# Kernel tuning notes

Measured on AMD Instinct MI355X. Metric: run time of the kernel, lower is better.

Reference implementation:

```python
import jax, jax.numpy as jnp
import numpy as np

C_Z = 128
C_H = 128
EPS = 1e-5


def _layer_norm(x, gamma, beta):
    mu = jnp.mean(x, axis=-1, keepdims=True)
    var = jnp.mean(jnp.square(x - mu), axis=-1, keepdims=True)
    return (x - mu) * jax.lax.rsqrt(var + EPS) * gamma + beta


def setup_inputs() -> dict:
    key = jax.random.key(0)
    ks = jax.random.split(key, 8)
    B, N = 1, 512
    s_z = 1.0 / np.sqrt(C_Z)
    s_h = 1.0 / np.sqrt(C_H)
    return {
        "z": jax.random.normal(ks[0], (B, N, N, C_Z), dtype=jnp.float32),
        "mask": jnp.ones((B, N, N), dtype=jnp.float32),
        # linear_ab_p: c_z -> 2*c_hidden
        "w_ab_p": jax.random.normal(ks[1], (2 * C_H, C_Z), dtype=jnp.float32) * s_z,
        "b_ab_p": jnp.zeros((2 * C_H,), dtype=jnp.float32),
        # linear_ab_g: c_z -> 2*c_hidden (gating init)
        "w_ab_g": jax.random.normal(ks[2], (2 * C_H, C_Z), dtype=jnp.float32) * s_z,
        "b_ab_g": jnp.ones((2 * C_H,), dtype=jnp.float32),
        # linear_g: c_z -> c_z (gating init)
        "w_g": jax.random.normal(ks[3], (C_Z, C_Z), dtype=jnp.float32) * s_z,
        "b_g": jnp.ones((C_Z,), dtype=jnp.float32),
        # linear_z: c_hidden -> c_z (final init)
        "w_z": jax.random.normal(ks[4], (C_Z, C_H), dtype=jnp.float32) * s_h,
        "b_z": jnp.zeros((C_Z,), dtype=jnp.float32),
        # layer norms
        "ln_in_g": jnp.ones((C_Z,), dtype=jnp.float32),
        "ln_in_b": jnp.zeros((C_Z,), dtype=jnp.float32),
        "ln_out_g": jnp.ones((C_H,), dtype=jnp.float32),
        "ln_out_b": jnp.zeros((C_H,), dtype=jnp.float32),
    }


def reference(z, mask, w_ab_p, b_ab_p, w_ab_g, b_ab_g, w_g, b_g, w_z, b_z,
              ln_in_g, ln_in_b, ln_out_g, ln_out_b):
    # [B, N, N, C] pair representation; outgoing triangle update
    zn = _layer_norm(z, ln_in_g, ln_in_b)
    m = mask[..., None]  # [B, N, N, 1]
    # gated dual projections: sigmoid(W_g z) * mask * (W_p z)  -> [B, N, N, 2H]
    gate = jax.nn.sigmoid(jnp.einsum("bijc,hc->bijh", zn, w_ab_g) + b_ab_g) * m
    ab = gate * (jnp.einsum("bijc,hc->bijh", zn, w_ab_p) + b_ab_p)
    a, b = jnp.split(ab, 2, axis=-1)  # each [B, N, N, H]
    # outgoing: x[b,i,j,h] = sum_k a[b,i,k,h] * b[b,j,k,h]
    x = jnp.einsum("bikh,bjkh->bijh", a, b)
    x = _layer_norm(x, ln_out_g, ln_out_b)
    out = (jnp.einsum("bijh,ch->bijc", x, w_z) + b_z)
    g = jax.nn.sigmoid(jnp.einsum("bijc,dc->bijd", zn, w_g) + b_g)
    return out * g
```

## Files before the change

### kernel.cpp

```cpp
#include <hip/hip_runtime.h>
#include <math.h>

#define NN 512
#define RR 262144
#define EPS_F 1e-5f

typedef unsigned short u16;
typedef unsigned int u32;
typedef __bf16 bf16x8 __attribute__((ext_vector_type(8)));
typedef float f32x4 __attribute__((ext_vector_type(4)));

__device__ __forceinline__ u16 f2bs(float f) {
  __bf16 h = (__bf16)f;
  return __builtin_bit_cast(u16, h);
}
__device__ __forceinline__ float bs2f(u16 u) {
  return (float)__builtin_bit_cast(__bf16, u);
}
__device__ __forceinline__ float sigmoidf_(float x) {
  return 1.f / (1.f + __expf(-x));
}

__global__ __launch_bounds__(256) void k_wconv(const float* __restrict__ w_ab_p,
                                               const float* __restrict__ w_ab_g,
                                               const float* __restrict__ w_g,
                                               u16* __restrict__ wb) {
  const int u = blockIdx.x * 256 + threadIdx.x;
  const int lane = u & 63;
  const int tl = lane & 15, quad = lane >> 4;
  const int ks = (u >> 6) & 3, nt = (u >> 8) & 3;
  const int wn = (u >> 10) & 1, tt = u >> 11;
  const int n = wn * 64 + nt * 16 + tl;
  const int k = ks * 32 + quad * 8;
  const float* src;
  if (tt < 4) {
    const int srow = tt * 64 + ((n >> 5) << 4) + (n & 15);
    src = (((n >> 4) & 1) ? w_ab_g : w_ab_p) + srow * 128 + k;
  } else {
    src = w_g + n * 128 + k;
  }
  const float4 v0 = *(const float4*)src;
  const float4 v1 = *(const float4*)(src + 4);
  u16 o[8] = {f2bs(v0.x), f2bs(v0.y), f2bs(v0.z), f2bs(v0.w),
              f2bs(v1.x), f2bs(v1.y), f2bs(v1.z), f2bs(v1.w)};
  *(uint4*)(wb + (long)u * 8) = *(uint4*)o;
}

__global__ __launch_bounds__(256, 3) void k_proj(
    const float* __restrict__ z, const float* __restrict__ mask,
    const u16* __restrict__ wb, const float* __restrict__ b_ab_p,
    const float* __restrict__ b_ab_g, const float* __restrict__ b_g,
    const float* __restrict__ ln_g, const float* __restrict__ ln_b,
    u16* __restrict__ a_t, u16* __restrict__ b_t, u16* __restrict__ g_out) {
  __shared__ __align__(16) u16 As[128 * 136];
  __shared__ __align__(16) u16 Ts[64 * 136];
  __shared__ float maskS[128];
  const int t = threadIdx.x;
  const long row0 = (long)blockIdx.x * 128;

  {
    const int row = t >> 1, half = t & 1;
    const float* zr = z + (row0 + row) * 128 + half * 64;
    float vals[64];
    float s = 0.f, sq = 0.f;
#pragma unroll
    for (int i = 0; i < 16; ++i) {
      const float4 v = *(const float4*)(zr + i * 4);
      vals[i * 4 + 0] = v.x;
      vals[i * 4 + 1] = v.y;
      vals[i * 4 + 2] = v.z;
      vals[i * 4 + 3] = v.w;
      s += v.x + v.y + v.z + v.w;
      sq += v.x * v.x + v.y * v.y + v.z * v.z + v.w * v.w;
    }
    s += __shfl_xor(s, 1);
    sq += __shfl_xor(sq, 1);
    const float mu = s * 0.0078125f;
    const float var = sq * 0.0078125f - mu * mu;
    const float rs = rsqrtf(var + EPS_F);
    u16 ob[64];
#pragma unroll
    for (int i = 0; i < 16; ++i) {
      const float4 gg = *(const float4*)(ln_g + half * 64 + i * 4);
      const float4 bb = *(const float4*)(ln_b + half * 64 + i * 4);
      ob[i * 4 + 0] = f2bs((vals[i * 4 + 0] - mu) * rs * gg.x + bb.x);
      ob[i * 4 + 1] = f2bs((vals[i * 4 + 1] - mu) * rs * gg.y + bb.y);
      ob[i * 4 + 2] = f2bs((vals[i * 4 + 2] - mu) * rs * gg.z + bb.z);
      ob[i * 4 + 3] = f2bs((vals[i * 4 + 3] - mu) * rs * gg.w + bb.w);
    }
    uint4* dst = (uint4*)(As + row * 136 + half * 64);
    const uint4* sp = (const uint4*)ob;
#pragma unroll
    for (int i = 0; i < 8; ++i) dst[i] = sp[i];
  }
  if (t < 128) maskS[t] = mask[row0 + t];
  __syncthreads();

  const int lane = t & 63, wv = t >> 6;
  const int quad = lane >> 4, tl = lane & 15;
  const int wm = wv >> 1, wn = wv & 1;

  for (int tt = 0; tt < 5; ++tt) {
    bf16x8 bfr[4][4];
    {
      const u16* wsrc = wb + (tt * 2 + wn) * 8192 + lane * 8;
#pragma unroll
      for (int nt = 0; nt < 4; ++nt)
#pragma unroll
        for (int ks = 0; ks < 4; ++ks)
          bfr[nt][ks] = *(const bf16x8*)(wsrc + (nt * 4 + ks) * 512);
    }

    f32x4 acc[4][4];
#pragma unroll
    for (int mt = 0; mt < 4; ++mt)
#pragma unroll
      for (int nt = 0; nt < 4; ++nt) acc[mt][nt] = (f32x4){0.f, 0.f, 0.f, 0.f};

#pragma unroll
    for (int ks = 0; ks < 4; ++ks) {
      bf16x8 af[4];
#pragma unroll
      for (int mt = 0; mt < 4; ++mt)
        af[mt] = *(const bf16x8*)(As + (wm * 64 + mt * 16 + tl) * 136 + ks * 32 + quad * 8);
#pragma unroll
      for (int mt = 0; mt < 4; ++mt)
#pragma unroll
        for (int nt = 0; nt < 4; ++nt)
          acc[mt][nt] = __builtin_amdgcn_mfma_f32_16x16x32_bf16(af[mt], bfr[nt][ks], acc[mt][nt], 0, 0, 0);
    }

    if (tt < 4) {
      __syncthreads();
#pragma unroll
      for (int b2 = 0; b2 < 2; ++b2) {
        const int hl = wn * 32 + b2 * 16 + tl;
        const int hg = tt * 64 + hl;
        const float bp = b_ab_p[hg], bg = b_ab_g[hg];
#pragma unroll
        for (int mt = 0; mt < 4; ++mt)
#pragma unroll
          for (int rg = 0; rg < 4; ++rg) {
            const int r = wm * 64 + mt * 16 + quad * 4 + rg;
            const float p = acc[mt][2 * b2][rg] + bp;
            const float gt = acc[mt][2 * b2 + 1][rg] + bg;
            Ts[hl * 136 + r] = f2bs(sigmoidf_(gt) * maskS[r] * p);
          }
      }
      __syncthreads();
      {
        const int hl = t >> 2, qq = t & 3;
        const int hg = tt * 64 + hl;
        u16* dbuf = (tt < 2) ? a_t : b_t;
        const int hb = (tt < 2) ? hg : hg - 128;
        const uint4* src = (const uint4*)(Ts + hl * 136 + qq * 32);
        uint4* dst = (uint4*)(dbuf + (long)hb * RR + row0 + qq * 32);
#pragma unroll
        for (int i = 0; i < 4; ++i) dst[i] = src[i];
      }
    } else {
#pragma unroll
      for (int nt = 0; nt < 4; ++nt) {
        const int c = wn * 64 + nt * 16 + tl;
        const float bgc = b_g[c];
#pragma unroll
        for (int mt = 0; mt < 4; ++mt)
#pragma unroll
          for (int rg = 0; rg < 4; ++rg) {
            const int r = wm * 64 + mt * 16 + quad * 4 + rg;
            g_out[(row0 + r) * (long)128 + c] = f2bs(sigmoidf_(acc[mt][nt][rg] + bgc));
          }
      }
    }
  }
}

__global__ __launch_bounds__(256) void k_tri(const u16* __restrict__ a_t,
                                             const u16* __restrict__ b_t,
                                             u16* __restrict__ x_t) {
  __shared__ __align__(16) u16 As[128 * 72];
  __shared__ __align__(16) u16 Bs[128 * 72];
  const int t = threadIdx.x;
  const int h = blockIdx.y;
  const int i0 = (blockIdx.x >> 2) * 128, j0 = (blockIdx.x & 3) * 128;
  const u16* Ag = a_t + (long)h * RR;
  const u16* Bg = b_t + (long)h * RR;
  const int lane = t & 63, wv = t >> 6;
  const int quad = lane >> 4, tl = lane & 15;
  const int wm = wv >> 1, wn = wv & 1;
  const int chunk = t & 7, rb = t >> 3;

  f32x4 acc[4][4];
#pragma unroll
  for (int mt = 0; mt < 4; ++mt)
#pragma unroll
    for (int nt = 0; nt < 4; ++nt) acc[mt][nt] = (f32x4){0.f, 0.f, 0.f, 0.f};

  for (int kt = 0; kt < 8; ++kt) {
    __syncthreads();
#pragma unroll
    for (int p = 0; p < 4; ++p) {
      const int row = rb + p * 32;
      *(uint4*)(As + row * 72 + chunk * 8) =
          *(const uint4*)(Ag + (long)(i0 + row) * 512 + kt * 64 + chunk * 8);
      *(uint4*)(Bs + row * 72 + chunk * 8) =
          *(const uint4*)(Bg + (long)(j0 + row) * 512 + kt * 64 + chunk * 8);
    }
    __syncthreads();
#pragma unroll
    for (int ks = 0; ks < 2; ++ks) {
      bf16x8 af[4], bfr[4];
#pragma unroll
      for (int mt = 0; mt < 4; ++mt)
        af[mt] = *(const bf16x8*)(As + (wm * 64 + mt * 16 + tl) * 72 + ks * 32 + quad * 8);
#pragma unroll
      for (int nt = 0; nt < 4; ++nt)
        bfr[nt] = *(const bf16x8*)(Bs + (wn * 64 + nt * 16 + tl) * 72 + ks * 32 + quad * 8);
#pragma unroll
      for (int mt = 0; mt < 4; ++mt)
#pragma unroll
        for (int nt = 0; nt < 4; ++nt)
          acc[mt][nt] = __builtin_amdgcn_mfma_f32_16x16x32_bf16(af[mt], bfr[nt], acc[mt][nt], 0, 0, 0);
    }
  }
#pragma unroll
  for (int mt = 0; mt < 4; ++mt)
#pragma unroll
    for (int nt = 0; nt < 4; ++nt)
#pragma unroll
      for (int rg = 0; rg < 4; ++rg) {
        const int i = i0 + wm * 64 + mt * 16 + quad * 4 + rg;
        const int j = j0 + wn * 64 + nt * 16 + tl;
        x_t[(long)h * RR + (long)i * 512 + j] = f2bs(acc[mt][nt][rg]);
      }
}

__global__ __launch_bounds__(256) void k_out(const u16* __restrict__ x_t,
                                             const float* __restrict__ w_z,
                                             const float* __restrict__ b_z,
                                             const float* __restrict__ ln_g,
                                             const float* __restrict__ ln_b,
                                             const u16* __restrict__ g_in,
                                             float* __restrict__ out) {
  __shared__ __align__(16) u16 Xs[128 * 136];
  __shared__ __align__(16) u16 Ws[128 * 136];
  __shared__ float lnGs[128], lnBs[128];
  const int t = threadIdx.x;
  const long row0 = (long)blockIdx.x * 128;

  if (t < 128) {
    lnGs[t] = ln_g[t];
    lnBs[t] = ln_b[t];
  }
  {
    const int hb = t >> 3, rq = t & 7;
    u32 xv[4][8];
#pragma unroll
    for (int hh = 0; hh < 4; ++hh) {
      const uint4* src = (const uint4*)(x_t + (long)(hb * 4 + hh) * RR + row0 + rq * 16);
      const uint4 a = src[0], b = src[1];
      xv[hh][0] = a.x; xv[hh][1] = a.y; xv[hh][2] = a.z; xv[hh][3] = a.w;
      xv[hh][4] = b.x; xv[hh][5] = b.y; xv[hh][6] = b.z; xv[hh][7] = b.w;
    }
#pragma unroll
    for (int rr = 0; rr < 16; ++rr) {
      const int wi = rr >> 1, sh = (rr & 1) * 16;
      const u32 e0 = (xv[0][wi] >> sh) & 0xffffu;
      const u32 e1 = (xv[1][wi] >> sh) & 0xffffu;
      const u32 e2 = (xv[2][wi] >> sh) & 0xffffu;
      const u32 e3 = (xv[3][wi] >> sh) & 0xffffu;
      *(uint2*)(Xs + (rq * 16 + rr) * 136 + hb * 4) = make_uint2(e0 | (e1 << 16), e2 | (e3 << 16));
    }
  }
  {
    const int n = t >> 1, half = t & 1;
    const float* src = w_z + n * 128 + half * 64;
    u16* dst = Ws + n * 136 + half * 64;
#pragma unroll
    for (int i = 0; i < 16; ++i) {
      const float4 v = *(const float4*)(src + i * 4);
      dst[i * 4 + 0] = f2bs(v.x);
      dst[i * 4 + 1] = f2bs(v.y);
      dst[i * 4 + 2] = f2bs(v.z);
      dst[i * 4 + 3] = f2bs(v.w);
    }
  }
  __syncthreads();
  {
    const int r = t >> 1, half = t & 1;
    u16* xr = Xs + r * 136 + half * 64;
    float vals[64];
    float s = 0.f, sq = 0.f;
#pragma unroll
    for (int i = 0; i < 64; ++i) {
      const float v = bs2f(xr[i]);
      vals[i] = v;
      s += v;
      sq += v * v;
    }
    s += __shfl_xor(s, 1);
    sq += __shfl_xor(sq, 1);
    const float mu = s * 0.0078125f;
    const float var = sq * 0.0078125f - mu * mu;
    const float rs = rsqrtf(var + EPS_F);
#pragma unroll
    for (int i = 0; i < 64; ++i) {
      const int hh = half * 64 + i;
      xr[i] = f2bs((vals[i] - mu) * rs * lnGs[hh] + lnBs[hh]);
    }
  }
  __syncthreads();

  const int lane = t & 63, wv = t >> 6;
  const int quad = lane >> 4, tl = lane & 15;
  const int wm = wv >> 1, wn = wv & 1;
  f32x4 acc[4][4];
#pragma unroll
  for (int mt = 0; mt < 4; ++mt)
#pragma unroll
    for (int nt = 0; nt < 4; ++nt) acc[mt][nt] = (f32x4){0.f, 0.f, 0.f, 0.f};

#pragma unroll
  for (int ks = 0; ks < 4; ++ks) {
    bf16x8 af[4], bfr[4];
#pragma unroll
    for (int mt = 0; mt < 4; ++mt)
      af[mt] = *(const bf16x8*)(Xs + (wm * 64 + mt * 16 + tl) * 136 + ks * 32 + quad * 8);
#pragma unroll
    for (int nt = 0; nt < 4; ++nt)
      bfr[nt] = *(const bf16x8*)(Ws + (wn * 64 + nt * 16 + tl) * 136 + ks * 32 + quad * 8);
#pragma unroll
    for (int mt = 0; mt < 4; ++mt)
#pragma unroll
      for (int nt = 0; nt < 4; ++nt)
        acc[mt][nt] = __builtin_amdgcn_mfma_f32_16x16x32_bf16(af[mt], bfr[nt], acc[mt][nt], 0, 0, 0);
  }
#pragma unroll
  for (int nt = 0; nt < 4; ++nt) {
    const int c = wn * 64 + nt * 16 + tl;
    const float bz = b_z[c];
#pragma unroll
    for (int mt = 0; mt < 4; ++mt)
#pragma unroll
      for (int rg = 0; rg < 4; ++rg) {
        const int r = wm * 64 + mt * 16 + quad * 4 + rg;
        const long idx = (row0 + r) * 128 + c;
        out[idx] = (acc[mt][nt][rg] + bz) * bs2f(g_in[idx]);
      }
  }
}

extern "C" void kernel_launch(void* const* d_in, const int* in_sizes, int n_in,
                              void* d_out, int out_size, void* d_ws, size_t ws_size,
                              hipStream_t stream) {
  const float* z = (const float*)d_in[0];
  const float* mask = (const float*)d_in[1];
  const float* w_ab_p = (const float*)d_in[2];
  const float* b_ab_p = (const float*)d_in[3];
  const float* w_ab_g = (const float*)d_in[4];
  const float* b_ab_g = (const float*)d_in[5];
  const float* w_g = (const float*)d_in[6];
  const float* b_g = (const float*)d_in[7];
  const float* w_z = (const float*)d_in[8];
  const float* b_z = (const float*)d_in[9];
  const float* ln_in_g = (const float*)d_in[10];
  const float* ln_in_b = (const float*)d_in[11];
  const float* ln_out_g = (const float*)d_in[12];
  const float* ln_out_b = (const float*)d_in[13];
  float* out = (float*)d_out;

  u16* a_t = (u16*)d_ws;
  u16* b_t = a_t + (size_t)RR * 128;
  u16* x_t = b_t + (size_t)RR * 128;
  u16* g_b = x_t + (size_t)RR * 128;
  u16* wb = g_b + (size_t)RR * 128;

  k_wconv<<<40, 256, 0, stream>>>(w_ab_p, w_ab_g, w_g, wb);
  k_proj<<<RR / 128, 256, 0, stream>>>(z, mask, wb, b_ab_p, b_ab_g, b_g,
                                       ln_in_g, ln_in_b, a_t, b_t, g_b);
  k_tri<<<dim3(16, 128), 256, 0, stream>>>(a_t, b_t, x_t);
  k_out<<<RR / 128, 256, 0, stream>>>(x_t, w_z, b_z, ln_out_g, ln_out_b, g_b, out);
}
```

Before: 493.2 us.

## Switch to fp16 MFMA, use direct global-to-LDS loads with XOR swizzle in triangle kernel

Result: no change. 491.9 us (-0.3%).

```diff
diff --git a/kernel.cpp b/kernel.cpp
--- a/kernel.cpp
+++ b/kernel.cpp
@@ -7,42 +7,57 @@
 
 typedef unsigned short u16;
 typedef unsigned int u32;
-typedef __bf16 bf16x8 __attribute__((ext_vector_type(8)));
+typedef _Float16 f16;
+typedef f16 f16x8 __attribute__((ext_vector_type(8)));
 typedef float f32x4 __attribute__((ext_vector_type(4)));
 
-__device__ __forceinline__ u16 f2bs(float f) {
-  __bf16 h = (__bf16)f;
+__device__ __forceinline__ u16 f2hs(float f) {
+  f16 h = (f16)f;
   return __builtin_bit_cast(u16, h);
 }
-__device__ __forceinline__ float bs2f(u16 u) {
-  return (float)__builtin_bit_cast(__bf16, u);
+__device__ __forceinline__ float hs2f(u16 u) {
+  return (float)__builtin_bit_cast(f16, u);
 }
 __device__ __forceinline__ float sigmoidf_(float x) {
   return 1.f / (1.f + __expf(-x));
+}
+__device__ __forceinline__ void gload_lds16(const void* g, void* l) {
+  __builtin_amdgcn_global_load_lds((const __attribute__((address_space(1))) void*)g,
+                                   (__attribute__((address_space(3))) void*)l, 16, 0, 0);
 }
 
 __global__ __launch_bounds__(256) void k_wconv(const float* __restrict__ w_ab_p,
                                                const float* __restrict__ w_ab_g,
                                                const float* __restrict__ w_g,
+                                               const float* __restrict__ w_z,
                                                u16* __restrict__ wb) {
   const int u = blockIdx.x * 256 + threadIdx.x;
-  const int lane = u & 63;
-  const int tl = lane & 15, quad = lane >> 4;
-  const int ks = (u >> 6) & 3, nt = (u >> 8) & 3;
-  const int wn = (u >> 10) & 1, tt = u >> 11;
-  const int n = wn * 64 + nt * 16 + tl;
-  const int k = ks * 32 + quad * 8;
   const float* src;
-  if (tt < 4) {
-    const int srow = tt * 64 + ((n >> 5) << 4) + (n & 15);
-    src = (((n >> 4) & 1) ? w_ab_g : w_ab_p) + srow * 128 + k;
+  if (u < 10240) {
+    const int lane = u & 63;
+    const int tl = lane & 15, quad = lane >> 4;
+    const int ks = (u >> 6) & 3, nt = (u >> 8) & 3;
+    const int wn = (u >> 10) & 1, tt = u >> 11;
+    const int n = wn * 64 + nt * 16 + tl;
+    const int k = ks * 32 + quad * 8;
+    if (tt < 4) {
+      const int srow = tt * 64 + ((n >> 5) << 4) + (n & 15);
+      src = (((n >> 4) & 1) ? w_ab_g : w_ab_p) + srow * 128 + k;
+    } else {
+      src = w_g + n * 128 + k;
+    }
   } else {
-    src = w_g + n * 128 + k;
+    const int u2 = u - 10240;
+    const int lane = u2 & 63;
+    const int ks = (u2 >> 6) & 3, nt = (u2 >> 8) & 3, wn = (u2 >> 10) & 1;
+    const int n = wn * 64 + nt * 16 + (lane & 15);
+    const int k = ks * 32 + (lane >> 4) * 8;
+    src = w_z + n * 128 + k;
   }
   const float4 v0 = *(const float4*)src;
   const float4 v1 = *(const float4*)(src + 4);
-  u16 o[8] = {f2bs(v0.x), f2bs(v0.y), f2bs(v0.z), f2bs(v0.w),
-              f2bs(v1.x), f2bs(v1.y), f2bs(v1.z), f2bs(v1.w)};
+  u16 o[8] = {f2hs(v0.x), f2hs(v0.y), f2hs(v0.z), f2hs(v0.w),
+              f2hs(v1.x), f2hs(v1.y), f2hs(v1.z), f2hs(v1.w)};
   *(uint4*)(wb + (long)u * 8) = *(uint4*)o;
 }
 
@@ -62,7 +77,7 @@
     const int row = t >> 1, half = t & 1;
     const float* zr = z + (row0 + row) * 128 + half * 64;
     float vals[64];
-    float s = 0.f, sq = 0.f;
+    float s = 0.f;
 #pragma unroll
     for (int i = 0; i < 16; ++i) {
       const float4 v = *(const float4*)(zr + i * 4);
@@ -71,22 +86,26 @@
       vals[i * 4 + 2] = v.z;
       vals[i * 4 + 3] = v.w;
       s += v.x + v.y + v.z + v.w;
-      sq += v.x * v.x + v.y * v.y + v.z * v.z + v.w * v.w;
     }
     s += __shfl_xor(s, 1);
+    const float mu = s * 0.0078125f;
+    float sq = 0.f;
+#pragma unroll
+    for (int i = 0; i < 64; ++i) {
+      const float d = vals[i] - mu;
+      sq += d * d;
+    }
     sq += __shfl_xor(sq, 1);
-    const float mu = s * 0.0078125f;
-    const float var = sq * 0.0078125f - mu * mu;
-    const float rs = rsqrtf(var + EPS_F);
+    const float rs = rsqrtf(sq * 0.0078125f + EPS_F);
     u16 ob[64];
 #pragma unroll
     for (int i = 0; i < 16; ++i) {
       const float4 gg = *(const float4*)(ln_g + half * 64 + i * 4);
       const float4 bb = *(const float4*)(ln_b + half * 64 + i * 4);
-      ob[i * 4 + 0] = f2bs((vals[i * 4 + 0] - mu) * rs * gg.x + bb.x);
-      ob[i * 4 + 1] = f2bs((vals[i * 4 + 1] - mu) * rs * gg.y + bb.y);
-      ob[i * 4 + 2] = f2bs((vals[i * 4 + 2] - mu) * rs * gg.z + bb.z);
-      ob[i * 4 + 3] = f2bs((vals[i * 4 + 3] - mu) * rs * gg.w + bb.w);
+      ob[i * 4 + 0] = f2hs((vals[i * 4 + 0] - mu) * rs * gg.x + bb.x);
+      ob[i * 4 + 1] = f2hs((vals[i * 4 + 1] - mu) * rs * gg.y + bb.y);
+      ob[i * 4 + 2] = f2hs((vals[i * 4 + 2] - mu) * rs * gg.z + bb.z);
+      ob[i * 4 + 3] = f2hs((vals[i * 4 + 3] - mu) * rs * gg.w + bb.w);
     }
     uint4* dst = (uint4*)(As + row * 136 + half * 64);
     const uint4* sp = (const uint4*)ob;
@@ -101,14 +120,14 @@
   const int wm = wv >> 1, wn = wv & 1;
 
   for (int tt = 0; tt < 5; ++tt) {
-    bf16x8 bfr[4][4];
+    f16x8 bfr[4][4];
     {
       const u16* wsrc = wb + (tt * 2 + wn) * 8192 + lane * 8;
 #pragma unroll
       for (int nt = 0; nt < 4; ++nt)
 #pragma unroll
         for (int ks = 0; ks < 4; ++ks)
-          bfr[nt][ks] = *(const bf16x8*)(wsrc + (nt * 4 + ks) * 512);
+          bfr[nt][ks] = *(const f16x8*)(wsrc + (nt * 4 + ks) * 512);
     }
 
     f32x4 acc[4][4];
@@ -119,15 +138,15 @@
 
 #pragma unroll
     for (int ks = 0; ks < 4; ++ks) {
-      bf16x8 af[4];
+      f16x8 af[4];
 #pragma unroll
       for (int mt = 0; mt < 4; ++mt)
-        af[mt] = *(const bf16x8*)(As + (wm * 64 + mt * 16 + tl) * 136 + ks * 32 + quad * 8);
+        af[mt] = *(const f16x8*)(As + (wm * 64 + mt * 16 + tl) * 136 + ks * 32 + quad * 8);
 #pragma unroll
       for (int mt = 0; mt < 4; ++mt)
 #pragma unroll
         for (int nt = 0; nt < 4; ++nt)
-          acc[mt][nt] = __builtin_amdgcn_mfma_f32_16x16x32_bf16(af[mt], bfr[nt][ks], acc[mt][nt], 0, 0, 0);
+          acc[mt][nt] = __builtin_amdgcn_mfma_f32_16x16x32_f16(af[mt], bfr[nt][ks], acc[mt][nt], 0, 0, 0);
     }
 
     if (tt < 4) {
@@ -144,7 +163,7 @@
             const int r = wm * 64 + mt * 16 + quad * 4 + rg;
             const float p = acc[mt][2 * b2][rg] + bp;
             const float gt = acc[mt][2 * b2 + 1][rg] + bg;
-            Ts[hl * 136 + r] = f2bs(sigmoidf_(gt) * maskS[r] * p);
+            Ts[hl * 136 + r] = f2hs(sigmoidf_(gt) * maskS[r] * p);
           }
       }
       __syncthreads();
@@ -168,27 +187,31 @@
 #pragma unroll
           for (int rg = 0; rg < 4; ++rg) {
             const int r = wm * 64 + mt * 16 + quad * 4 + rg;
-            g_out[(row0 + r) * (long)128 + c] = f2bs(sigmoidf_(acc[mt][nt][rg] + bgc));
+            g_out[(row0 + r) * (long)128 + c] = f2hs(sigmoidf_(acc[mt][nt][rg] + bgc));
           }
       }
     }
   }
 }
 
-__global__ __launch_bounds__(256) void k_tri(const u16* __restrict__ a_t,
-                                             const u16* __restrict__ b_t,
-                                             u16* __restrict__ x_t) {
-  __shared__ __align__(16) u16 As[128 * 72];
-  __shared__ __align__(16) u16 Bs[128 * 72];
+__global__ __launch_bounds__(256, 4) void k_tri(const u16* __restrict__ a_t,
+                                                const u16* __restrict__ b_t,
+                                                u16* __restrict__ x_t) {
+  __shared__ __align__(16) u16 As[128 * 64];
+  __shared__ __align__(16) u16 Bs[128 * 64];
   const int t = threadIdx.x;
-  const int h = blockIdx.y;
-  const int i0 = (blockIdx.x >> 2) * 128, j0 = (blockIdx.x & 3) * 128;
+  const int bid = blockIdx.x;
+  const int swz = (bid & 7) * 256 + (bid >> 3);
+  const int h = swz >> 4;
+  const int i0 = ((swz >> 2) & 3) * 128, j0 = (swz & 3) * 128;
   const u16* Ag = a_t + (long)h * RR;
   const u16* Bg = b_t + (long)h * RR;
   const int lane = t & 63, wv = t >> 6;
   const int quad = lane >> 4, tl = lane & 15;
   const int wm = wv >> 1, wn = wv & 1;
-  const int chunk = t & 7, rb = t >> 3;
+  const int lrow = lane >> 3;
+  const int lu = lane & 7;
+  const int su = lu ^ lrow;
 
   f32x4 acc[4][4];
 #pragma unroll
@@ -197,30 +220,35 @@
     for (int nt = 0; nt < 4; ++nt) acc[mt][nt] = (f32x4){0.f, 0.f, 0.f, 0.f};
 
   for (int kt = 0; kt < 8; ++kt) {
+    if (kt) __syncthreads();
+#pragma unroll
+    for (int it = 0; it < 4; ++it) {
+      const int rbase = wv * 32 + it * 8;
+      const int r = rbase + lrow;
+      gload_lds16(Ag + (long)(i0 + r) * 512 + kt * 64 + su * 8, As + rbase * 64);
+      gload_lds16(Bg + (long)(j0 + r) * 512 + kt * 64 + su * 8, Bs + rbase * 64);
+    }
     __syncthreads();
 #pragma unroll
-    for (int p = 0; p < 4; ++p) {
-      const int row = rb + p * 32;
-      *(uint4*)(As + row * 72 + chunk * 8) =
-          *(const uint4*)(Ag + (long)(i0 + row) * 512 + kt * 64 + chunk * 8);
-      *(uint4*)(Bs + row * 72 + chunk * 8) =
-          *(const uint4*)(Bg + (long)(j0 + row) * 512 + kt * 64 + chunk * 8);
-    }
-    __syncthreads();
-#pragma unroll
     for (int ks = 0; ks < 2; ++ks) {
-      bf16x8 af[4], bfr[4];
+      f16x8 af[4], bfr[4];
+#pragma unroll
+      for (int mt = 0; mt < 4; ++mt) {
+        const int row = wm * 64 + mt * 16 + tl;
+        const int unit = (ks * 4 + quad) ^ (row & 7);
+        af[mt] = *(const f16x8*)(As + row * 64 + unit * 8);
+      }
+#pragma unroll
+      for (int nt = 0; nt < 4; ++nt) {
+        const int row = wn * 64 + nt * 16 + tl;
+        const int unit = (ks * 4 + quad) ^ (row & 7);
+        bfr[nt] = *(const f16x8*)(Bs + row * 64 + unit * 8);
+      }
 #pragma unroll
       for (int mt = 0; mt < 4; ++mt)
-        af[mt] = *(const bf16x8*)(As + (wm * 64 + mt * 16 + tl) * 72 + ks * 32 + quad * 8);
-#pragma unroll
-      for (int nt = 0; nt < 4; ++nt)
-        bfr[nt] = *(const bf16x8*)(Bs + (wn * 64 + nt * 16 + tl) * 72 + ks * 32 + quad * 8);
-#pragma unroll
-      for (int mt = 0; mt < 4; ++mt)
 #pragma unroll
         for (int nt = 0; nt < 4; ++nt)
-          acc[mt][nt] = __builtin_amdgcn_mfma_f32_16x16x32_bf16(af[mt], bfr[nt], acc[mt][nt], 0, 0, 0);
+          acc[mt][nt] = __builtin_amdgcn_mfma_f32_16x16x32_f16(af[mt], bfr[nt], acc[mt][nt], 0, 0, 0);
     }
   }
 #pragma unroll
@@ -231,19 +259,18 @@
       for (int rg = 0; rg < 4; ++rg) {
         const int i = i0 + wm * 64 + mt * 16 + quad * 4 + rg;
         const int j = j0 + wn * 64 + nt * 16 + tl;
-        x_t[(long)h * RR + (long)i * 512 + j] = f2bs(acc[mt][nt][rg]);
-      }
-}
-
-__global__ __launch_bounds__(256) void k_out(const u16* __restrict__ x_t,
-                                             const float* __restrict__ w_z,
-                                             const float* __restrict__ b_z,
-                                             const float* __restrict__ ln_g,
-                                             const float* __restrict__ ln_b,
-                                             const u16* __restrict__ g_in,
-                                             float* __restrict__ out) {
+        x_t[(long)h * RR + (long)i * 512 + j] = f2hs(acc[mt][nt][rg]);
+      }
+}
+
+__global__ __launch_bounds__(256, 4) void k_out(const u16* __restrict__ x_t,
+                                                const u16* __restrict__ wb,
+                                                const float* __restrict__ b_z,
+                                                const float* __restrict__ ln_g,
+                                                const float* __restrict__ ln_b,
+                                                const u16* __restrict__ g_in,
+                                                float* __restrict__ out) {
   __shared__ __align__(16) u16 Xs[128 * 136];
-  __shared__ __align__(16) u16 Ws[128 * 136];
   __shared__ float lnGs[128], lnBs[128];
   const int t = threadIdx.x;
   const long row0 = (long)blockIdx.x * 128;
@@ -272,41 +299,41 @@
       *(uint2*)(Xs + (rq * 16 + rr) * 136 + hb * 4) = make_uint2(e0 | (e1 << 16), e2 | (e3 << 16));
     }
   }
-  {
-    const int n = t >> 1, half = t & 1;
-    const float* src = w_z + n * 128 + half * 64;
-    u16* dst = Ws + n * 136 + half * 64;
-#pragma unroll
-    for (int i = 0; i < 16; ++i) {
-      const float4 v = *(const float4*)(src + i * 4);
-      dst[i * 4 + 0] = f2bs(v.x);
-      dst[i * 4 + 1] = f2bs(v.y);
-      dst[i * 4 + 2] = f2bs(v.z);
-      dst[i * 4 + 3] = f2bs(v.w);
-    }
-  }
   __syncthreads();
   {
     const int r = t >> 1, half = t & 1;
     u16* xr = Xs + r * 136 + half * 64;
-    float vals[64];
-    float s = 0.f, sq = 0.f;
-#pragma unroll
-    for (int i = 0; i < 64; ++i) {
-      const float v = bs2f(xr[i]);
-      vals[i] = v;
-      s += v;
-      sq += v * v;
+    float s = 0.f;
+#pragma unroll
+    for (int i = 0; i < 8; ++i) {
+      const f16x8 v = *(const f16x8*)(xr + i * 8);
+#pragma unroll
+      for (int j = 0; j < 8; ++j) s += (float)v[j];
     }
     s += __shfl_xor(s, 1);
+    const float mu = s * 0.0078125f;
+    float sq = 0.f;
+#pragma unroll
+    for (int i = 0; i < 8; ++i) {
+      const f16x8 v = *(const f16x8*)(xr + i * 8);
+#pragma unroll
+      for (int j = 0; j < 8; ++j) {
+        const float d = (float)v[j] - mu;
+        sq += d * d;
+      }
+    }
     sq += __shfl_xor(sq, 1);
-    const float mu = s * 0.0078125f;
-    const float var = sq * 0.0078125f - mu * mu;
-    const float rs = rsqrtf(var + EPS_F);
-#pragma unroll
-    for (int i = 0; i < 64; ++i) {
-      const int hh = half * 64 + i;
-      xr[i] = f2bs((vals[i] - mu) * rs * lnGs[hh] + lnBs[hh]);
+    const float rs = rsqrtf(sq * 0.0078125f + EPS_F);
+#pragma unroll
+    for (int i = 0; i < 8; ++i) {
+      const f16x8 v = *(const f16x8*)(xr + i * 8);
+      u16 ob[8];
+#pragma unroll
+      for (int j = 0; j < 8; ++j) {
+        const int hh = half * 64 + i * 8 + j;
+        ob[j] = f2hs(((float)v[j] - mu) * rs * lnGs[hh] + lnBs[hh]);
+      }
+      *(uint4*)(xr + i * 8) = *(uint4*)ob;
     }
   }
   __syncthreads();
@@ -320,20 +347,21 @@
 #pragma unroll
     for (int nt = 0; nt < 4; ++nt) acc[mt][nt] = (f32x4){0.f, 0.f, 0.f, 0.f};
 
+  const u16* wzb = wb + 81920 + wn * 8192 + lane * 8;
 #pragma unroll
   for (int ks = 0; ks < 4; ++ks) {
-    bf16x8 af[4], bfr[4];
+    f16x8 af[4], bfr[4];
+#pragma unroll
+    for (int nt = 0; nt < 4; ++nt)
+      bfr[nt] = *(const f16x8*)(wzb + (nt * 4 + ks) * 512);
 #pragma unroll
     for (int mt = 0; mt < 4; ++mt)
-      af[mt] = *(const bf16x8*)(Xs + (wm * 64 + mt * 16 + tl) * 136 + ks * 32 + quad * 8);
-#pragma unroll
-    for (int nt = 0; nt < 4; ++nt)
-      bfr[nt] = *(const bf16x8*)(Ws + (wn * 64 + nt * 16 + tl) * 136 + ks * 32 + quad * 8);
+      af[mt] = *(const f16x8*)(Xs + (wm * 64 + mt * 16 + tl) * 136 + ks * 32 + quad * 8);
 #pragma unroll
     for (int mt = 0; mt < 4; ++mt)
 #pragma unroll
       for (int nt = 0; nt < 4; ++nt)
-        acc[mt][nt] = __builtin_amdgcn_mfma_f32_16x16x32_bf16(af[mt], bfr[nt], acc[mt][nt], 0, 0, 0);
+        acc[mt][nt] = __builtin_amdgcn_mfma_f32_16x16x32_f16(af[mt], bfr[nt], acc[mt][nt], 0, 0, 0);
   }
 #pragma unroll
   for (int nt = 0; nt < 4; ++nt) {
@@ -345,7 +373,7 @@
       for (int rg = 0; rg < 4; ++rg) {
         const int r = wm * 64 + mt * 16 + quad * 4 + rg;
         const long idx = (row0 + r) * 128 + c;
-        out[idx] = (acc[mt][nt][rg] + bz) * bs2f(g_in[idx]);
+        out[idx] = (acc[mt][nt][rg] + bz) * hs2f(g_in[idx]);
       }
   }
 }
@@ -375,9 +403,9 @@
   u16* g_b = x_t + (size_t)RR * 128;
   u16* wb = g_b + (size_t)RR * 128;
 
-  k_wconv<<<40, 256, 0, stream>>>(w_ab_p, w_ab_g, w_g, wb);
+  k_wconv<<<48, 256, 0, stream>>>(w_ab_p, w_ab_g, w_g, w_z, wb);
   k_proj<<<RR / 128, 256, 0, stream>>>(z, mask, wb, b_ab_p, b_ab_g, b_g,
                                        ln_in_g, ln_in_b, a_t, b_t, g_b);
-  k_tri<<<dim3(16, 128), 256, 0, stream>>>(a_t, b_t, x_t);
-  k_out<<<RR / 128, 256, 0, stream>>>(x_t, w_z, b_z, ln_out_g, ln_out_b, g_b, out);
-}
+  k_tri<<<2048, 256, 0, stream>>>(a_t, b_t, x_t);
+  k_out<<<RR / 128, 256, 0, stream>>>(x_t, wb, b_z, ln_out_g, ln_out_b, g_b, out);
+}
```
